# Kernel optimization log

Hardware: AMD Instinct MI355X
Metric: run time of the kernel (lower is better)

Reference implementation:

```python
import jax, jax.numpy as jnp
import numpy as np

N, K, DIN, DOUT = 100000, 32, 128, 64
NEG = -9e15  # sentinel written into row 0 before the neighbor gather


def setup_inputs() -> dict:
    key = jax.random.key(0)
    k1, k2, k3, k4 = jax.random.split(key, 4)
    x = jax.random.normal(k1, (N, DIN), dtype=jnp.float32)
    a2a = jax.random.randint(k2, (N, K), 0, N, dtype=jnp.int64)
    W = jax.random.normal(k3, (DOUT, DIN), dtype=jnp.float32) * (1.0 / np.sqrt(DIN))
    b = jax.random.normal(k4, (DOUT,), dtype=jnp.float32) * 0.01
    return {"x": x, "a2a": a2a, "W": W, "b": b}


def reference(x, a2a, W, b):
    # h = Linear(x); row 0 overwritten with the -9e15 padding sentinel
    h = x @ W.T + b                                   # [N, DOUT]
    h = h.at[0].set(NEG)
    # attention logits: bmm(cat([h, h[a2a]], dim=1), h) without materializing the concat
    self_dot = jnp.sum(h * h, axis=-1, keepdims=True)  # [N, 1]
    nbr = h[a2a]                                       # [N, K, DOUT] gather
    nbr_dot = jnp.einsum('nkd,nd->nk', nbr, h)         # [N, K]
    logits = jnp.concatenate([self_dot, nbr_dot], axis=1)  # [N, K+1]
    att = jax.nn.softmax(logits, axis=1)
    out = h * att[:, 0:1]                              # scale by self-attention weight
    out = out.at[0].set(0.0)
    return out
```

## Files before the change

kernel.cpp:

```cpp
#include <hip/hip_runtime.h>

#define NN   100000
#define KK   32
#define DIN  128
#define DOUT 64
#define NEGV (-9e15f)

typedef __attribute__((ext_vector_type(8))) short bf16x8;
typedef __attribute__((ext_vector_type(4))) float f32x4;

__device__ __forceinline__ float bflo(unsigned u) { return __uint_as_float(u << 16); }
__device__ __forceinline__ float bfhi(unsigned u) { return __uint_as_float(u & 0xffff0000u); }
__device__ __forceinline__ ushort f2bf(float f) {
    unsigned u = __float_as_uint(f);
    return (ushort)((u + 0x7fffu + ((u >> 16) & 1u)) >> 16);
}
__device__ __forceinline__ unsigned pk2(float a, float b) {
    unsigned r;
    asm("v_cvt_pk_bf16_f32 %0, %1, %2" : "=v"(r) : "v"(a), "v"(b));
    return r;
}
__device__ __forceinline__ bf16x8 cvt8(float4 a, float4 b) {
    union { unsigned u[4]; bf16x8 v; } r;
    r.u[0] = pk2(a.x, a.y); r.u[1] = pk2(a.z, a.w);
    r.u[2] = pk2(b.x, b.y); r.u[3] = pk2(b.z, b.w);
    return r.v;
}

__global__ __launch_bounds__(256) void h_kernel(const float* __restrict__ x,
                                                const float* __restrict__ W,
                                                const float* __restrict__ b,
                                                ushort* __restrict__ hb) {
    const int t    = threadIdx.x;
    const int w    = t >> 6;
    const int lane = t & 63;
    const int lr   = lane & 15;
    const int lg   = lane >> 4;

    bf16x8 Bf[4][4];
    const float* wp = W + (size_t)lr * DIN + lg * 8;
#pragma unroll
    for (int ct = 0; ct < 4; ++ct)
#pragma unroll
        for (int ks = 0; ks < 4; ++ks) {
            const float* p = wp + ct * 16 * DIN + ks * 32;
            Bf[ct][ks] = cvt8(*(const float4*)p, *(const float4*)(p + 4));
        }

    float bias[4];
#pragma unroll
    for (int ct = 0; ct < 4; ++ct) bias[ct] = b[ct * 16 + lr];

    const int base = blockIdx.x * 128 + w * 16;
#pragma unroll
    for (int tile = 0; tile < 2; ++tile) {
        const int row0 = base + tile * 64;

        int ar = row0 + lr;
        if (ar > NN - 1) ar = NN - 1;
        const float* xp = x + (size_t)ar * DIN + lg * 8;

        bf16x8 Af[4];
#pragma unroll
        for (int ks = 0; ks < 4; ++ks)
            Af[ks] = cvt8(*(const float4*)(xp + ks * 32),
                          *(const float4*)(xp + ks * 32 + 4));

        f32x4 acc[4] = {{0.f,0.f,0.f,0.f},{0.f,0.f,0.f,0.f},
                        {0.f,0.f,0.f,0.f},{0.f,0.f,0.f,0.f}};
#pragma unroll
        for (int ct = 0; ct < 4; ++ct)
#pragma unroll
            for (int ks = 0; ks < 4; ++ks)
                acc[ct] = __builtin_amdgcn_mfma_f32_16x16x32_bf16(
                    Af[ks], Bf[ct][ks], acc[ct], 0, 0, 0);

#pragma unroll
        for (int ct = 0; ct < 4; ++ct)
#pragma unroll
            for (int j = 0; j < 4; ++j) {
                const int m = row0 + lg * 4 + j;
                if (m < NN) {
                    const float v = (m == 0) ? NEGV : (acc[ct][j] + bias[ct]);
                    hb[(size_t)m * DOUT + ct * 16 + lr] = f2bf(v);
                }
            }
    }
}

__global__ __launch_bounds__(256) void att_kernel(const ushort* __restrict__ hb,
                                                  const int* __restrict__ a2a,
                                                  float* __restrict__ out) {
    const int t    = threadIdx.x;
    const int wid  = t >> 6;
    const int lane = t & 63;
    const int lr   = lane & 15;
    const int lg   = lane >> 4;
    const int n0   = blockIdx.x * 8 + wid * 2;

#pragma unroll
    for (int r = 0; r < 2; ++r) {
        const int n = n0 + r;
        const ushort* hbn = hb + (size_t)n * DOUT;

        const bf16x8 B0 = *(const bf16x8*)(hbn + lg * 8);
        const bf16x8 B1 = *(const bf16x8*)(hbn + 32 + lg * 8);

        const int i0 = a2a[n * KK + lr];
        const int i1 = a2a[n * KK + 16 + lr];
        const ushort* p0 = hb + (size_t)i0 * DOUT + lg * 8;
        const ushort* p1 = hb + (size_t)i1 * DOUT + lg * 8;

        const bf16x8 A00 = *(const bf16x8*)p0;
        const bf16x8 A01 = *(const bf16x8*)(p0 + 32);
        const bf16x8 A10 = *(const bf16x8*)p1;
        const bf16x8 A11 = *(const bf16x8*)(p1 + 32);

        const float hv = bflo((unsigned)hbn[lane]);

        f32x4 d0 = {0.f, 0.f, 0.f, 0.f};
        f32x4 d1 = {0.f, 0.f, 0.f, 0.f};
        d0 = __builtin_amdgcn_mfma_f32_16x16x32_bf16(A00, B0, d0, 0, 0, 0);
        d0 = __builtin_amdgcn_mfma_f32_16x16x32_bf16(A01, B1, d0, 0, 0, 0);
        d1 = __builtin_amdgcn_mfma_f32_16x16x32_bf16(A10, B0, d1, 0, 0, 0);
        d1 = __builtin_amdgcn_mfma_f32_16x16x32_bf16(A11, B1, d1, 0, 0, 0);

        union { bf16x8 v; unsigned u[4]; } ub0, ub1;
        ub0.v = B0; ub1.v = B1;
        float sp = 0.f;
#pragma unroll
        for (int i = 0; i < 4; ++i) {
            float a = bflo(ub0.u[i]), c = bfhi(ub0.u[i]);
            float e = bflo(ub1.u[i]), g = bfhi(ub1.u[i]);
            sp = fmaf(a, a, sp); sp = fmaf(c, c, sp);
            sp = fmaf(e, e, sp); sp = fmaf(g, g, sp);
        }
        sp += __shfl_xor(sp, 16);
        sp += __shfl_xor(sp, 32);

        float m = fmaxf(fmaxf(fmaxf(d0[0], d0[1]), fmaxf(d0[2], d0[3])),
                        fmaxf(fmaxf(d1[0], d1[1]), fmaxf(d1[2], d1[3])));
        m = fmaxf(m, __shfl_xor(m, 16));
        m = fmaxf(m, __shfl_xor(m, 32));
        m = fmaxf(m, sp);

        float s = __expf(d0[0] - m) + __expf(d0[1] - m) +
                  __expf(d0[2] - m) + __expf(d0[3] - m) +
                  __expf(d1[0] - m) + __expf(d1[1] - m) +
                  __expf(d1[2] - m) + __expf(d1[3] - m);
        s += __shfl_xor(s, 16);
        s += __shfl_xor(s, 32);

        const float es = __expf(sp - m);
        const float w0 = es / (es + s);

        float o = hv * w0;
        if (n == 0) o = 0.f;
        out[(size_t)n * DOUT + lane] = o;
    }
}

extern "C" void kernel_launch(void* const* d_in, const int* in_sizes, int n_in,
                              void* d_out, int out_size, void* d_ws, size_t ws_size,
                              hipStream_t stream) {
    const float* x   = (const float*)d_in[0];
    const int*   a2a = (const int*)d_in[1];
    const float* W   = (const float*)d_in[2];
    const float* b   = (const float*)d_in[3];
    float*       out = (float*)d_out;
    ushort*      hb  = (ushort*)d_ws;

    h_kernel<<<(NN + 127) / 128, 256, 0, stream>>>(x, W, b, hb);
    att_kernel<<<NN / 8, 256, 0, stream>>>(hb, a2a, out);
}
```

Measured before the change: 169.8 us.

## Pre-convert x to bf16 in a separate pass and give each att wave one node

Adds a grid-stride kernel that converts x to bf16 into workspace; the linear kernel then loads bf16 rows instead of converting fp32 in place. The old fp32 linear kernel stays as a fallback when the workspace is too small. The attention kernel now handles one node per wave instead of two, which doubles the grid size. The extra pass reads x in full and writes it back at half size, so total memory traffic rises, and whether it runs depends on ws_size.

```diff
diff --git a/kernel.cpp b/kernel.cpp
--- a/kernel.cpp
+++ b/kernel.cpp
@@ -27,10 +27,25 @@
     return r.v;
 }
 
-__global__ __launch_bounds__(256) void h_kernel(const float* __restrict__ x,
-                                                const float* __restrict__ W,
-                                                const float* __restrict__ b,
-                                                ushort* __restrict__ hb) {
+__global__ __launch_bounds__(256) void x2b_kernel(const float* __restrict__ x,
+                                                  ushort* __restrict__ xb) {
+    const int total = NN * DIN / 4;
+    const float4* xp = reinterpret_cast<const float4*>(x);
+    uint2* op = reinterpret_cast<uint2*>(xb);
+    for (int i = blockIdx.x * blockDim.x + threadIdx.x; i < total;
+         i += gridDim.x * blockDim.x) {
+        const float4 v = xp[i];
+        uint2 o;
+        o.x = pk2(v.x, v.y);
+        o.y = pk2(v.z, v.w);
+        op[i] = o;
+    }
+}
+
+__global__ __launch_bounds__(256) void h_kernel_bf16(const ushort* __restrict__ xb,
+                                                     const float* __restrict__ W,
+                                                     const float* __restrict__ b,
+                                                     ushort* __restrict__ hb) {
     const int t    = threadIdx.x;
     const int w    = t >> 6;
     const int lane = t & 63;
@@ -56,6 +71,65 @@
     for (int tile = 0; tile < 2; ++tile) {
         const int row0 = base + tile * 64;
 
+        int ar = row0 + lr;
+        if (ar > NN - 1) ar = NN - 1;
+        const ushort* xp = xb + (size_t)ar * DIN + lg * 8;
+
+        bf16x8 Af[4];
+#pragma unroll
+        for (int ks = 0; ks < 4; ++ks)
+            Af[ks] = *(const bf16x8*)(xp + ks * 32);
+
+        f32x4 acc[4] = {{0.f,0.f,0.f,0.f},{0.f,0.f,0.f,0.f},
+                        {0.f,0.f,0.f,0.f},{0.f,0.f,0.f,0.f}};
+#pragma unroll
+        for (int ct = 0; ct < 4; ++ct)
+#pragma unroll
+            for (int ks = 0; ks < 4; ++ks)
+                acc[ct] = __builtin_amdgcn_mfma_f32_16x16x32_bf16(
+                    Af[ks], Bf[ct][ks], acc[ct], 0, 0, 0);
+
+#pragma unroll
+        for (int ct = 0; ct < 4; ++ct)
+#pragma unroll
+            for (int j = 0; j < 4; ++j) {
+                const int m = row0 + lg * 4 + j;
+                if (m < NN) {
+                    const float v = (m == 0) ? NEGV : (acc[ct][j] + bias[ct]);
+                    hb[(size_t)m * DOUT + ct * 16 + lr] = f2bf(v);
+                }
+            }
+    }
+}
+
+__global__ __launch_bounds__(256) void h_kernel_f32(const float* __restrict__ x,
+                                                    const float* __restrict__ W,
+                                                    const float* __restrict__ b,
+                                                    ushort* __restrict__ hb) {
+    const int t    = threadIdx.x;
+    const int w    = t >> 6;
+    const int lane = t & 63;
+    const int lr   = lane & 15;
+    const int lg   = lane >> 4;
+
+    bf16x8 Bf[4][4];
+    const float* wp = W + (size_t)lr * DIN + lg * 8;
+#pragma unroll
+    for (int ct = 0; ct < 4; ++ct)
+#pragma unroll
+        for (int ks = 0; ks < 4; ++ks) {
+            const float* p = wp + ct * 16 * DIN + ks * 32;
+            Bf[ct][ks] = cvt8(*(const float4*)p, *(const float4*)(p + 4));
+        }
+
+    float bias[4];
+#pragma unroll
+    for (int ct = 0; ct < 4; ++ct) bias[ct] = b[ct * 16 + lr];
+
+    const int base = blockIdx.x * 128 + w * 16;
+#pragma unroll
+    for (int tile = 0; tile < 2; ++tile) {
+        const int row0 = base + tile * 64;
         int ar = row0 + lr;
         if (ar > NN - 1) ar = NN - 1;
         const float* xp = x + (size_t)ar * DIN + lg * 8;
@@ -96,68 +170,63 @@
     const int lane = t & 63;
     const int lr   = lane & 15;
     const int lg   = lane >> 4;
-    const int n0   = blockIdx.x * 8 + wid * 2;
-
-#pragma unroll
-    for (int r = 0; r < 2; ++r) {
-        const int n = n0 + r;
-        const ushort* hbn = hb + (size_t)n * DOUT;
-
-        const bf16x8 B0 = *(const bf16x8*)(hbn + lg * 8);
-        const bf16x8 B1 = *(const bf16x8*)(hbn + 32 + lg * 8);
-
-        const int i0 = a2a[n * KK + lr];
-        const int i1 = a2a[n * KK + 16 + lr];
-        const ushort* p0 = hb + (size_t)i0 * DOUT + lg * 8;
-        const ushort* p1 = hb + (size_t)i1 * DOUT + lg * 8;
-
-        const bf16x8 A00 = *(const bf16x8*)p0;
-        const bf16x8 A01 = *(const bf16x8*)(p0 + 32);
-        const bf16x8 A10 = *(const bf16x8*)p1;
-        const bf16x8 A11 = *(const bf16x8*)(p1 + 32);
-
-        const float hv = bflo((unsigned)hbn[lane]);
-
-        f32x4 d0 = {0.f, 0.f, 0.f, 0.f};
-        f32x4 d1 = {0.f, 0.f, 0.f, 0.f};
-        d0 = __builtin_amdgcn_mfma_f32_16x16x32_bf16(A00, B0, d0, 0, 0, 0);
-        d0 = __builtin_amdgcn_mfma_f32_16x16x32_bf16(A01, B1, d0, 0, 0, 0);
-        d1 = __builtin_amdgcn_mfma_f32_16x16x32_bf16(A10, B0, d1, 0, 0, 0);
-        d1 = __builtin_amdgcn_mfma_f32_16x16x32_bf16(A11, B1, d1, 0, 0, 0);
-
-        union { bf16x8 v; unsigned u[4]; } ub0, ub1;
-        ub0.v = B0; ub1.v = B1;
-        float sp = 0.f;
-#pragma unroll
-        for (int i = 0; i < 4; ++i) {
-            float a = bflo(ub0.u[i]), c = bfhi(ub0.u[i]);
-            float e = bflo(ub1.u[i]), g = bfhi(ub1.u[i]);
-            sp = fmaf(a, a, sp); sp = fmaf(c, c, sp);
-            sp = fmaf(e, e, sp); sp = fmaf(g, g, sp);
-        }
-        sp += __shfl_xor(sp, 16);
-        sp += __shfl_xor(sp, 32);
-
-        float m = fmaxf(fmaxf(fmaxf(d0[0], d0[1]), fmaxf(d0[2], d0[3])),
-                        fmaxf(fmaxf(d1[0], d1[1]), fmaxf(d1[2], d1[3])));
-        m = fmaxf(m, __shfl_xor(m, 16));
-        m = fmaxf(m, __shfl_xor(m, 32));
-        m = fmaxf(m, sp);
-
-        float s = __expf(d0[0] - m) + __expf(d0[1] - m) +
-                  __expf(d0[2] - m) + __expf(d0[3] - m) +
-                  __expf(d1[0] - m) + __expf(d1[1] - m) +
-                  __expf(d1[2] - m) + __expf(d1[3] - m);
-        s += __shfl_xor(s, 16);
-        s += __shfl_xor(s, 32);
-
-        const float es = __expf(sp - m);
-        const float w0 = es / (es + s);
-
-        float o = hv * w0;
-        if (n == 0) o = 0.f;
-        out[(size_t)n * DOUT + lane] = o;
-    }
+    const int n    = blockIdx.x * 4 + wid;
+
+    const ushort* hbn = hb + (size_t)n * DOUT;
+
+    const int i0 = a2a[n * KK + lr];
+    const int i1 = a2a[n * KK + 16 + lr];
+    const ushort* p0 = hb + (size_t)i0 * DOUT + lg * 8;
+    const ushort* p1 = hb + (size_t)i1 * DOUT + lg * 8;
+
+    const bf16x8 A00 = *(const bf16x8*)p0;
+    const bf16x8 A01 = *(const bf16x8*)(p0 + 32);
+    const bf16x8 A10 = *(const bf16x8*)p1;
+    const bf16x8 A11 = *(const bf16x8*)(p1 + 32);
+
+    const bf16x8 B0 = *(const bf16x8*)(hbn + lg * 8);
+    const bf16x8 B1 = *(const bf16x8*)(hbn + 32 + lg * 8);
+    const float hv = bflo((unsigned)hbn[lane]);
+
+    f32x4 d0 = {0.f, 0.f, 0.f, 0.f};
+    f32x4 d1 = {0.f, 0.f, 0.f, 0.f};
+    d0 = __builtin_amdgcn_mfma_f32_16x16x32_bf16(A00, B0, d0, 0, 0, 0);
+    d0 = __builtin_amdgcn_mfma_f32_16x16x32_bf16(A01, B1, d0, 0, 0, 0);
+    d1 = __builtin_amdgcn_mfma_f32_16x16x32_bf16(A10, B0, d1, 0, 0, 0);
+    d1 = __builtin_amdgcn_mfma_f32_16x16x32_bf16(A11, B1, d1, 0, 0, 0);
+
+    union { bf16x8 v; unsigned u[4]; } ub0, ub1;
+    ub0.v = B0; ub1.v = B1;
+    float sp = 0.f;
+#pragma unroll
+    for (int i = 0; i < 4; ++i) {
+        float a = bflo(ub0.u[i]), c = bfhi(ub0.u[i]);
+        float e = bflo(ub1.u[i]), g = bfhi(ub1.u[i]);
+        sp = fmaf(a, a, sp); sp = fmaf(c, c, sp);
+        sp = fmaf(e, e, sp); sp = fmaf(g, g, sp);
+    }
+    sp += __shfl_xor(sp, 16);
+    sp += __shfl_xor(sp, 32);
+
+    float m = fmaxf(fmaxf(fmaxf(d0[0], d0[1]), fmaxf(d0[2], d0[3])),
+                    fmaxf(fmaxf(d1[0], d1[1]), fmaxf(d1[2], d1[3])));
+    m = fmaxf(m, __shfl_xor(m, 16));
+    m = fmaxf(m, __shfl_xor(m, 32));
+    m = fmaxf(m, sp);
+
+    float s = __expf(d0[0] - m) + __expf(d0[1] - m) +
+              __expf(d0[2] - m) + __expf(d0[3] - m) +
+              __expf(d1[0] - m) + __expf(d1[1] - m) +
+              __expf(d1[2] - m) + __expf(d1[3] - m);
+    s += __shfl_xor(s, 16);
+    s += __shfl_xor(s, 32);
+
+    const float es = __expf(sp - m);
+    const float w0 = es / (es + s);
+
+    float o = hv * w0;
+    if (n == 0) o = 0.f;
+    out[(size_t)n * DOUT + lane] = o;
 }
 
 extern "C" void kernel_launch(void* const* d_in, const int* in_sizes, int n_in,
@@ -168,8 +237,17 @@
     const float* W   = (const float*)d_in[2];
     const float* b   = (const float*)d_in[3];
     float*       out = (float*)d_out;
-    ushort*      hb  = (ushort*)d_ws;
-
-    h_kernel<<<(NN + 127) / 128, 256, 0, stream>>>(x, W, b, hb);
-    att_kernel<<<NN / 8, 256, 0, stream>>>(hb, a2a, out);
-}
+
+    const size_t hb_bytes = (size_t)NN * DOUT * 2;
+    const size_t need     = hb_bytes + (size_t)NN * DIN * 2;
+    ushort* hb = (ushort*)d_ws;
+
+    if (ws_size >= need) {
+        ushort* xb = (ushort*)((char*)d_ws + hb_bytes);
+        x2b_kernel<<<2048, 256, 0, stream>>>(x, xb);
+        h_kernel_bf16<<<(NN + 127) / 128, 256, 0, stream>>>(xb, W, b, hb);
+    } else {
+        h_kernel_f32<<<(NN + 127) / 128, 256, 0, stream>>>(x, W, b, hb);
+    }
+    att_kernel<<<NN / 4, 256, 0, stream>>>(hb, a2a, out);
+}
```

Result: slower. 178.3 us (+5.0%).
